# Kernel optimization log

Hardware: AMD Instinct MI355X
Metric: run time of the kernel (lower is better)

The kernel has to match this reference:

```python
import jax, jax.numpy as jnp
import numpy as np

N, E, D, H, FF = 50000, 800000, 128, 8, 512
DK = D // H
NTYPES = 5
EPS = 1e-5


def setup_inputs() -> dict:
    key = jax.random.key(0)
    ks = jax.random.split(key, 8)
    x = jax.random.normal(ks[0], (N, D), jnp.float32)
    edges = jax.random.randint(ks[1], (2, E), 0, N)
    etype = jax.random.randint(ks[2], (E,), 0, NTYPES)
    masks = etype[None, :] == jnp.arange(NTYPES)[:, None]  # [5, E] bool, exact partition
    s = 1.0 / np.sqrt(D)
    Wk = jax.random.normal(ks[3], (NTYPES, D, D), jnp.float32) * s
    bk = jnp.zeros((NTYPES, D), jnp.float32)
    ln1_g = jnp.ones((D,), jnp.float32)
    ln1_b = jnp.zeros((D,), jnp.float32)
    ln2_g = jnp.ones((D,), jnp.float32)
    ln2_b = jnp.zeros((D,), jnp.float32)
    W1 = jax.random.normal(ks[4], (D, FF), jnp.float32) * s
    b1 = jnp.zeros((FF,), jnp.float32)
    W2 = jax.random.normal(ks[5], (FF, D), jnp.float32) * (1.0 / np.sqrt(FF))
    b2 = jnp.zeros((D,), jnp.float32)
    return {"x": x, "edges": edges, "masks": masks, "Wk": Wk, "bk": bk,
            "ln1_g": ln1_g, "ln1_b": ln1_b, "ln2_g": ln2_g, "ln2_b": ln2_b,
            "W1": W1, "b1": b1, "W2": W2, "b2": b2}


def _layernorm(x, g, b):
    mu = x.mean(-1, keepdims=True)
    var = x.var(-1, keepdims=True)
    return (x - mu) * jax.lax.rsqrt(var + EPS) * g + b


def _proj(z, idx, masks, W, b):
    # per-edge-type masked linear: output[mask_i] = x[idx[mask_i]] @ W_i + b_i
    g = z[idx]  # [E, D] gather
    out = jnp.zeros((g.shape[0], D), z.dtype)
    for i in range(NTYPES):
        out = out + jnp.where(masks[i][:, None], g @ W[i] + b[i], 0.0)
    return out.reshape(-1, H, DK)  # [E, H, d_k]


def reference(x, edges, masks, Wk, bk, ln1_g, ln1_b, ln2_g, ln2_b, W1, b1, W2, b2):
    src, dst = edges[0], edges[1]
    n = x.shape[0]
    z = _layernorm(x, ln1_g, ln1_b)
    # source module uses self.key projection for query, key AND value
    q = _proj(z, src, masks, Wk, bk)   # [E, H, d_k]
    k = _proj(z, dst, masks, Wk, bk)   # [E, H, d_k]
    v = k                              # value = key(z, edges[1]) == key, reuse
    logits = (q * k).sum(2, keepdims=True)  # [E, H, 1], unscaled as in source
    m = jax.ops.segment_max(jax.lax.stop_gradient(logits), src, num_segments=n)
    scores = jnp.exp(logits - m[src])
    den = jax.ops.segment_sum(scores, src, num_segments=n)
    scores = scores / den[src]
    attn = jax.ops.segment_sum(scores * v, src, num_segments=n).reshape(n, -1)  # [N, D]
    x = x + attn
    z2 = _layernorm(x, ln2_g, ln2_b)
    ff = jax.nn.relu(z2 @ W1 + b1) @ W2 + b2
    return x + ff
```

## Files before the change

### kernel.cpp

```cpp
#include <hip/hip_runtime.h>

#define D 128
#define H 8
#define DK 16
#define FFDIM 512
#define NTYPES 5
#define LN_EPS 1e-5f

typedef __bf16 bf16x8 __attribute__((ext_vector_type(8)));
typedef float f32x4 __attribute__((ext_vector_type(4)));
typedef unsigned short ushort_t;
typedef unsigned int uint_t;

__device__ inline ushort_t bfbits(float f) {
  __bf16 b = (__bf16)f;
  return __builtin_bit_cast(ushort_t, b);
}

__global__ void detect_kernel(const unsigned char* __restrict__ m8, int E,
                              int* __restrict__ flag) {
  int lane = threadIdx.x;
  int s = 1;
  if (lane < E) {
    s = 0;
#pragma unroll
    for (int i = 0; i < NTYPES; ++i) s += (m8[(size_t)i * E + lane] != 0);
  }
  unsigned long long b = __ballot(s == 1);
  if (lane == 0) *flag = (b == ~0ull) ? 1 : 0;
}

__device__ inline int decode_etype(const unsigned char* __restrict__ m8,
                                   int E, int e, int is8) {
  int t = 0;
  if (is8) {
#pragma unroll
    for (int i = 1; i < NTYPES; ++i) t += i * (m8[(size_t)i * E + e] != 0);
  } else {
    const int* m32 = (const int*)m8;
#pragma unroll
    for (int i = 1; i < NTYPES; ++i) t += i * (m32[(size_t)i * E + e] != 0);
  }
  return t > (NTYPES - 1) ? (NTYPES - 1) : t;
}

__global__ void conv_frag_kernel(const float* __restrict__ W,
                                 ushort_t* __restrict__ hi,
                                 int K, int Ncol, size_t matW, size_t matF) {
  int gid = blockIdx.x * 256 + threadIdx.x;
  int total = (Ncol / 16) * (K / 32) * 64;
  if (gid >= total) return;
  const float* Wm = W + (size_t)blockIdx.y * matW;
  ushort_t* him = hi + (size_t)blockIdx.y * matF;
  int l = gid & 63;
  int ck = gid >> 6;
  int kk = ck % (K / 32);
  int c = ck / (K / 32);
  int row0 = kk * 32 + (l >> 4) * 8;
  int col = c * 16 + (l & 15);
  size_t ob = (size_t)gid * 8;
#pragma unroll
  for (int j = 0; j < 8; ++j) {
    float w = Wm[(size_t)(row0 + j) * Ncol + col];
    __bf16 h = (__bf16)w;
    him[ob + j] = __builtin_bit_cast(ushort_t, h);
  }
}

__global__ __launch_bounds__(256, 4) void projln_kernel(
    const float* __restrict__ x, const float* __restrict__ g,
    const float* __restrict__ b, const ushort_t* __restrict__ wkh,
    const float* __restrict__ bk, ushort_t* __restrict__ P, int n) {
  __shared__ ushort_t zsh[64 * D];
  __shared__ ushort_t zsl[64 * D];
  int tid = threadIdx.x, w = tid >> 6, l = tid & 63;
  int n0 = blockIdx.x * 64;

  for (int i = w; i < 64; i += 4) {
    int r = n0 + i;
    float v0 = 0.f, v1 = 0.f;
    if (r < n) {
      v0 = x[(size_t)r * D + l];
      v1 = x[(size_t)r * D + 64 + l];
    }
    float s = v0 + v1, ss = v0 * v0 + v1 * v1;
    for (int o = 32; o; o >>= 1) { s += __shfl_xor(s, o); ss += __shfl_xor(ss, o); }
    float mu = s * (1.f / D);
    float var = ss * (1.f / D) - mu * mu;
    float rs = rsqrtf(var + LN_EPS);
    float z0 = (v0 - mu) * rs * g[l] + b[l];
    float z1 = (v1 - mu) * rs * g[l + 64] + b[l + 64];
    int sw = (i & 7) << 3;
    int e0 = (i * D + l) ^ sw;
    int e1 = (i * D + l + 64) ^ sw;
    __bf16 h0 = (__bf16)z0, h1 = (__bf16)z1;
    zsh[e0] = __builtin_bit_cast(ushort_t, h0);
    zsh[e1] = __builtin_bit_cast(ushort_t, h1);
    __bf16 l0 = (__bf16)(z0 - (float)h0), l1 = (__bf16)(z1 - (float)h1);
    zsl[e0] = __builtin_bit_cast(ushort_t, l0);
    zsl[e1] = __builtin_bit_cast(ushort_t, l1);
  }
  __syncthreads();

  int lrow = w * 16 + (l & 15);
  int koff = (l >> 4) * 8;
  bf16x8 ah[4], al[4];
#pragma unroll
  for (int kk = 0; kk < 4; ++kk) {
    int e = (lrow * D + kk * 32 + koff) ^ ((lrow & 7) << 3);
    ah[kk] = *(const bf16x8*)(zsh + e);
    al[kk] = *(const bf16x8*)(zsl + e);
  }

  int col16 = l & 15, rgrp = (l >> 4) * 4;
  int rowbase = n0 + w * 16;
  for (int t = 0; t < NTYPES; ++t) {
    const ushort_t* bh0 = wkh + (size_t)t * (D * D);
    ushort_t* Pt = P + (size_t)t * n * D;
#pragma unroll
    for (int cp = 0; cp < 4; ++cp) {
      bf16x8 Bh[2][4];
#pragma unroll
      for (int cc = 0; cc < 2; ++cc)
#pragma unroll
        for (int kk = 0; kk < 4; ++kk) {
          size_t o = ((size_t)((cp * 2 + cc) * 4 + kk) * 64 + l) * 8;
          Bh[cc][kk] = *(const bf16x8*)(bh0 + o);
        }
      f32x4 aa[2], ac[2];
#pragma unroll
      for (int cc = 0; cc < 2; ++cc) {
        float bias = bk[t * D + (cp * 2 + cc) * 16 + col16];
        aa[cc] = (f32x4){bias, bias, bias, bias};
        ac[cc] = (f32x4){0.f, 0.f, 0.f, 0.f};
      }
#pragma unroll
      for (int kk = 0; kk < 4; ++kk)
#pragma unroll
        for (int cc = 0; cc < 2; ++cc) {
          aa[cc] = __builtin_amdgcn_mfma_f32_16x16x32_bf16(ah[kk], Bh[cc][kk], aa[cc], 0, 0, 0);
          ac[cc] = __builtin_amdgcn_mfma_f32_16x16x32_bf16(al[kk], Bh[cc][kk], ac[cc], 0, 0, 0);
        }
#pragma unroll
      for (int cc = 0; cc < 2; ++cc)
#pragma unroll
        for (int r = 0; r < 4; ++r) {
          int row = rowbase + rgrp + r;
          if (row < n)
            Pt[(size_t)row * D + (cp * 2 + cc) * 16 + col16] =
                bfbits(aa[cc][r] + ac[cc][r]);
        }
    }
  }
}

__global__ void zero_kernel(int* __restrict__ p, int n) {
  int i = blockIdx.x * 256 + threadIdx.x;
  if (i < n) p[i] = 0;
}

__global__ void hist5_kernel(const int* __restrict__ edges,
                             const unsigned char* __restrict__ masks,
                             const int* __restrict__ flag,
                             int* __restrict__ cnt5,
                             unsigned char* __restrict__ etype8, int E) {
  int e = blockIdx.x * 256 + threadIdx.x;
  if (e >= E) return;
  int t = decode_etype(masks, E, e, *flag);
  etype8[e] = (unsigned char)t;
  atomicAdd(&cnt5[edges[e] * 8 + t], 1);
}

__global__ __launch_bounds__(256) void scanA5_kernel(const int* __restrict__ cnt5,
                                                     int* __restrict__ loc,
                                                     int* __restrict__ bsums, int n) {
  __shared__ int ts[256];
  int tid = threadIdx.x;
  int i = blockIdx.x * 256 + tid;
  int v = 0;
  if (i < n) {
    int4 c0 = *(const int4*)(cnt5 + (size_t)i * 8);
    v = c0.x + c0.y + c0.z + c0.w + cnt5[(size_t)i * 8 + 4];
  }
  ts[tid] = v;
  __syncthreads();
  for (int o = 1; o < 256; o <<= 1) {
    int t = (tid >= o) ? ts[tid - o] : 0;
    __syncthreads();
    ts[tid] += t;
    __syncthreads();
  }
  if (i < n) loc[i] = ts[tid] - v;
  if (tid == 255) bsums[blockIdx.x] = ts[255];
}

__global__ __launch_bounds__(256) void scanB_kernel(int* __restrict__ bsums, int nb,
                                                    int* __restrict__ total) {
  __shared__ int ts[256];
  int tid = threadIdx.x;
  int per = (nb + 255) / 256;
  int start = tid * per;
  int end = min(start + per, nb);
  int s = 0;
  for (int i = start; i < end; ++i) s += bsums[i];
  ts[tid] = s;
  __syncthreads();
  for (int o = 1; o < 256; o <<= 1) {
    int t = (tid >= o) ? ts[tid - o] : 0;
    __syncthreads();
    ts[tid] += t;
    __syncthreads();
  }
  int run = ts[tid] - s;
  for (int i = start; i < end; ++i) {
    int v = bsums[i];
    bsums[i] = run;
    run += v;
  }
  if (tid == 255) *total = ts[255];
}

__global__ void build5_kernel(const int* __restrict__ loc,
                              const int* __restrict__ bsums,
                              const int* __restrict__ cnt5,
                              int* __restrict__ cursor5, int* __restrict__ tb,
                              int n) {
  int i = blockIdx.x * 256 + threadIdx.x;
  if (i >= n) return;
  int base = loc[i] + bsums[i >> 8];
#pragma unroll
  for (int t = 0; t < NTYPES; ++t) {
    int c = cnt5[(size_t)i * 8 + t];
    cursor5[(size_t)i * 8 + t] = base;
    tb[(size_t)i * 8 + t] = base;
    base += c;
  }
  tb[(size_t)i * 8 + 5] = base;
}

__global__ __launch_bounds__(256) void fill_kernel(
    const int* __restrict__ edges, const unsigned char* __restrict__ etype8,
    int* __restrict__ cursor5, int* __restrict__ elist, int E, int n) {
  int bx = blockIdx.x;
  int range = bx & 7;
  int e = (bx >> 3) * 256 + threadIdx.x;
  if (e >= E) return;
  int per = (n + 7) >> 3;
  int lo = range * per;
  int hi = min(lo + per, n);
  int src = edges[e];
  if (src < lo || src >= hi) return;
  int t = etype8[e];
  int dst = edges[E + e];
  int pos = atomicAdd(&cursor5[src * 8 + t], 1);
  elist[pos] = t * n + dst;
}

__global__ __launch_bounds__(256, 4) void attn_kernel(
    const float* __restrict__ x, const ushort_t* __restrict__ P,
    const int* __restrict__ tb, const int* __restrict__ elist,
    float* __restrict__ out, int n) {
  int node = (blockIdx.x * 256 + threadIdx.x) >> 4;
  int gl = threadIdx.x & 15;
  if (node >= n) return;

  int4 t03 = *(const int4*)(tb + (size_t)node * 8);
  int2 t45 = *(const int2*)(tb + (size_t)node * 8 + 4);
  int bnd0 = t03.x, bnd1 = t03.y, bnd2 = t03.z, bnd3 = t03.w;
  int bnd4 = t45.x, bnd5 = t45.y;

  float m = -1e30f, den = 0.f;
  float a[8];
#pragma unroll
  for (int i = 0; i < 8; ++i) a[i] = 0.f;

#pragma unroll
  for (int t = 0; t < NTYPES; ++t) {
    int jb = (t == 0) ? bnd0 : (t == 1) ? bnd1 : (t == 2) ? bnd2
             : (t == 3) ? bnd3 : bnd4;
    int je = (t == 0) ? bnd1 : (t == 1) ? bnd2 : (t == 2) ? bnd3
             : (t == 3) ? bnd4 : bnd5;
    if (jb >= je) continue;
    bf16x8 qb = *(const bf16x8*)(P + (size_t)(t * n + node) * D + gl * 8);
    float qf[8];
#pragma unroll
    for (int d = 0; d < 8; ++d) qf[d] = (float)qb[d];

    int row = elist[jb];
    bf16x8 kv = *(const bf16x8*)(P + (size_t)row * D + gl * 8);
    for (int j = jb; j < je; ++j) {
      bf16x8 kvn = kv;
      if (j + 1 < je) {
        int rn = elist[j + 1];
        kvn = *(const bf16x8*)(P + (size_t)rn * D + gl * 8);
      }
      float kf[8], p = 0.f;
#pragma unroll
      for (int d = 0; d < 8; ++d) {
        kf[d] = (float)kv[d];
        p += qf[d] * kf[d];
      }
      p += __shfl_xor(p, 1);
      float nm = fmaxf(m, p);
      float sc = __expf(m - nm);
      float w = __expf(p - nm);
      den = den * sc + w;
#pragma unroll
      for (int d = 0; d < 8; ++d) a[d] = a[d] * sc + w * kf[d];
      m = nm;
      kv = kvn;
    }
  }

  float inv = (bnd5 > bnd0) ? 1.f / den : 0.f;
  const float* xr = x + (size_t)node * D + gl * 8;
  float* orow = out + (size_t)node * D + gl * 8;
  float4 xa = *(const float4*)xr;
  float4 xb = *(const float4*)(xr + 4);
  float4 oa, ob;
  oa.x = xa.x + a[0] * inv; oa.y = xa.y + a[1] * inv;
  oa.z = xa.z + a[2] * inv; oa.w = xa.w + a[3] * inv;
  ob.x = xb.x + a[4] * inv; ob.y = xb.y + a[5] * inv;
  ob.z = xb.z + a[6] * inv; ob.w = xb.w + a[7] * inv;
  *(float4*)orow = oa;
  *(float4*)(orow + 4) = ob;
}

__global__ __launch_bounds__(256, 4) void ffn_mfma_kernel(
    const ushort_t* __restrict__ w1h, const ushort_t* __restrict__ w2h,
    const float* __restrict__ b1, const float* __restrict__ b2,
    const float* __restrict__ g, const float* __restrict__ bln,
    float* __restrict__ out, int n) {
  __shared__ char smem[16640 + 4 * 2304];
  ushort_t* z2h = (ushort_t*)smem;
  ushort_t* z2l = (ushort_t*)(smem + 8192);
  float* red = (float*)smem;
  int tid = threadIdx.x, w = tid >> 6, l = tid & 63;
  int n0 = blockIdx.x * 32;
  int r2 = w & 1, ph = w >> 1;
  float* hbw = (float*)(smem + 16640) + w * 576;

  for (int i = w; i < 32; i += 4) {
    int r = n0 + i;
    float v0 = 0.f, v1 = 0.f;
    if (r < n) {
      v0 = out[(size_t)r * D + l];
      v1 = out[(size_t)r * D + 64 + l];
    }
    float s = v0 + v1, ss = v0 * v0 + v1 * v1;
    for (int o = 32; o; o >>= 1) { s += __shfl_xor(s, o); ss += __shfl_xor(ss, o); }
    float mu = s * (1.f / D);
    float var = ss * (1.f / D) - mu * mu;
    float rs = rsqrtf(var + LN_EPS);
    float z0 = (v0 - mu) * rs * g[l] + bln[l];
    float z1 = (v1 - mu) * rs * g[l + 64] + bln[l + 64];
    int sw = (i & 7) << 3;
    int e0 = (i * D + l) ^ sw;
    int e1 = (i * D + l + 64) ^ sw;
    __bf16 h0 = (__bf16)z0, h1 = (__bf16)z1;
    z2h[e0] = __builtin_bit_cast(ushort_t, h0);
    z2h[e1] = __builtin_bit_cast(ushort_t, h1);
    __bf16 l0 = (__bf16)(z0 - (float)h0), l1 = (__bf16)(z1 - (float)h1);
    z2l[e0] = __builtin_bit_cast(ushort_t, l0);
    z2l[e1] = __builtin_bit_cast(ushort_t, l1);
  }
  __syncthreads();

  int lrow = r2 * 16 + (l & 15);
  int koff = (l >> 4) * 8;
  bf16x8 ah[4], al[4];
#pragma unroll
  for (int kk = 0; kk < 4; ++kk) {
    int e = (lrow * D + kk * 32 + koff) ^ ((lrow & 7) << 3);
    ah[kk] = *(const bf16x8*)(z2h + e);
    al[kk] = *(const bf16x8*)(z2l + e);
  }
  __syncthreads();

  int col16 = l & 15, rgrp = (l >> 4) * 4;
  f32x4 acc2[8];
#pragma unroll
  for (int c = 0; c < 8; ++c) acc2[c] = (f32x4){0.f, 0.f, 0.f, 0.f};

  for (int i = 0; i < 8; ++i) {
    int kk2 = 2 * i + ph;
    bf16x8 B1h[2][4];
#pragma unroll
    for (int cc = 0; cc < 2; ++cc)
#pragma unroll
      for (int kk = 0; kk < 4; ++kk) {
        size_t o = ((size_t)((kk2 * 2 + cc) * 4 + kk) * 64 + l) * 8;
        B1h[cc][kk] = *(const bf16x8*)(w1h + o);
      }
    f32x4 ha[2], hc[2];
#pragma unroll
    for (int cc = 0; cc < 2; ++cc) {
      float bias = b1[(kk2 * 2 + cc) * 16 + col16];
      ha[cc] = (f32x4){bias, bias, bias, bias};
      hc[cc] = (f32x4){0.f, 0.f, 0.f, 0.f};
    }
#pragma unroll
    for (int kk = 0; kk < 4; ++kk)
#pragma unroll
      for (int cc = 0; cc < 2; ++cc) {
        ha[cc] = __builtin_amdgcn_mfma_f32_16x16x32_bf16(ah[kk], B1h[cc][kk], ha[cc], 0, 0, 0);
        hc[cc] = __builtin_amdgcn_mfma_f32_16x16x32_bf16(al[kk], B1h[cc][kk], hc[cc], 0, 0, 0);
      }
#pragma unroll
    for (int cc = 0; cc < 2; ++cc)
#pragma unroll
      for (int r = 0; r < 4; ++r)
        hbw[(rgrp + r) * 36 + cc * 16 + col16] = fmaxf(ha[cc][r] + hc[cc][r], 0.f);
    float av[8];
    *(float4*)&av[0] = *(const float4*)&hbw[(l & 15) * 36 + koff];
    *(float4*)&av[4] = *(const float4*)&hbw[(l & 15) * 36 + koff + 4];
    bf16x8 a2h, a2l;
#pragma unroll
    for (int j = 0; j < 8; ++j) {
      __bf16 hv = (__bf16)av[j];
      a2h[j] = hv;
      a2l[j] = (__bf16)(av[j] - (float)hv);
    }
#pragma unroll
    for (int half = 0; half < 2; ++half) {
      bf16x8 B2h[4];
#pragma unroll
      for (int c2 = 0; c2 < 4; ++c2) {
        int ct = half * 4 + c2;
        size_t o = ((size_t)(ct * 16 + kk2) * 64 + l) * 8;
        B2h[c2] = *(const bf16x8*)(w2h + o);
      }
#pragma unroll
      for (int c2 = 0; c2 < 4; ++c2) {
        int ct = half * 4 + c2;
        acc2[ct] = __builtin_amdgcn_mfma_f32_16x16x32_bf16(a2h, B2h[c2], acc2[ct], 0, 0, 0);
        acc2[ct] = __builtin_amdgcn_mfma_f32_16x16x32_bf16(a2l, B2h[c2], acc2[ct], 0, 0, 0);
      }
    }
  }

  if (ph == 0) {
#pragma unroll
    for (int ct = 0; ct < 8; ++ct)
#pragma unroll
      for (int r = 0; r < 4; ++r)
        red[(r2 * 16 + rgrp + r) * 130 + ct * 16 + col16] = acc2[ct][r];
  }
  __syncthreads();
  if (ph == 1) {
#pragma unroll
    for (int ct = 0; ct < 8; ++ct) {
      int col = ct * 16 + col16;
      float bias2 = b2[col];
#pragma unroll
      for (int r = 0; r < 4; ++r) {
        int row = n0 + r2 * 16 + rgrp + r;
        if (row < n) {
          float part = red[(r2 * 16 + rgrp + r) * 130 + col];
          size_t o = (size_t)row * D + col;
          out[o] = out[o] + acc2[ct][r] + part + bias2;
        }
      }
    }
  }
}

extern "C" void kernel_launch(void* const* d_in, const int* in_sizes, int n_in,
                              void* d_out, int out_size, void* d_ws, size_t ws_size,
                              hipStream_t stream) {
  const float* x      = (const float*)d_in[0];
  const int* edges    = (const int*)d_in[1];
  const unsigned char* masks = (const unsigned char*)d_in[2];
  const float* Wk     = (const float*)d_in[3];
  const float* bk     = (const float*)d_in[4];
  const float* ln1_g  = (const float*)d_in[5];
  const float* ln1_b  = (const float*)d_in[6];
  const float* ln2_g  = (const float*)d_in[7];
  const float* ln2_b  = (const float*)d_in[8];
  const float* W1     = (const float*)d_in[9];
  const float* b1     = (const float*)d_in[10];
  const float* W2     = (const float*)d_in[11];
  const float* b2     = (const float*)d_in[12];
  float* out = (float*)d_out;

  const int n = in_sizes[0] / D;
  const int E = in_sizes[1] / 2;
  const int nbn = (n + 255) / 256;

  char* ws = (char*)d_ws;
  size_t off = 0;
  ushort_t* P = (ushort_t*)(ws + off);  off += (size_t)NTYPES * n * D * sizeof(ushort_t);
  int* cnt5   = (int*)(ws + off);       off += (size_t)n * 8 * sizeof(int);
  int* cursor5= (int*)(ws + off);       off += (size_t)n * 8 * sizeof(int);
  int* tb     = (int*)(ws + off);       off += (size_t)n * 8 * sizeof(int);
  int* loc    = (int*)(ws + off);       off += (size_t)n * sizeof(int);
  int* bsums  = (int*)(ws + off);       off += (size_t)nbn * sizeof(int);
  int* total  = (int*)(ws + off);       off += 64;
  int* elist  = (int*)(ws + off);       off += (size_t)E * sizeof(int);
  unsigned char* etype8 = (unsigned char*)(ws + off); off += (size_t)E + 64;
  int* flag   = (int*)(ws + off);       off += 64;
  ushort_t* wkh = (ushort_t*)(ws + off); off += (size_t)NTYPES * D * D * sizeof(ushort_t);
  ushort_t* w1h = (ushort_t*)(ws + off); off += (size_t)D * FFDIM * sizeof(ushort_t);
  ushort_t* w2h = (ushort_t*)(ws + off); off += (size_t)FFDIM * D * sizeof(ushort_t);
  (void)ws_size; (void)n_in; (void)out_size;

  detect_kernel<<<1, 64, 0, stream>>>(masks, E, flag);

  {
    dim3 gwk((8 * 4 * 64 + 255) / 256, NTYPES);
    conv_frag_kernel<<<gwk, 256, 0, stream>>>(Wk, wkh, D, D,
                                              (size_t)D * D, (size_t)D * D);
    dim3 gw1(((FFDIM / 16) * 4 * 64 + 255) / 256, 1);
    conv_frag_kernel<<<gw1, 256, 0, stream>>>(W1, w1h, D, FFDIM, 0, 0);
    dim3 gw2((8 * (FFDIM / 32) * 64 + 255) / 256, 1);
    conv_frag_kernel<<<gw2, 256, 0, stream>>>(W2, w2h, FFDIM, D, 0, 0);
  }

  projln_kernel<<<(n + 63) / 64, 256, 0, stream>>>(x, ln1_g, ln1_b, wkh, bk, P, n);

  zero_kernel<<<(n * 8 + 255) / 256, 256, 0, stream>>>(cnt5, n * 8);
  hist5_kernel<<<(E + 255) / 256, 256, 0, stream>>>(edges, masks, flag, cnt5, etype8, E);
  scanA5_kernel<<<nbn, 256, 0, stream>>>(cnt5, loc, bsums, n);
  scanB_kernel<<<1, 256, 0, stream>>>(bsums, nbn, total);
  build5_kernel<<<(n + 255) / 256, 256, 0, stream>>>(loc, bsums, cnt5, cursor5, tb, n);
  fill_kernel<<<((E + 255) / 256) * 8, 256, 0, stream>>>(edges, etype8, cursor5,
                                                         elist, E, n);

  attn_kernel<<<(n + 15) / 16, 256, 0, stream>>>(x, P, tb, elist, out, n);

  ffn_mfma_kernel<<<(n + 31) / 32, 256, 0, stream>>>(w1h, w2h,
                                                     b1, b2, ln2_g, ln2_b, out, n);
}
```

Baseline: 244.0 us.

## Drop bf16 split-precision in FFN and range-partition the edge histogram

The FFN kernel no longer splits the LayerNorm and ReLU activations into high and low bf16 halves. It runs a single bf16 MFMA per tile, which halves the matrix-core work and removes some shared-memory traffic. Separately, edge-type decoding moves into its own kernel, and the histogram is launched with 8 times as many blocks, each handling only the edges whose source node falls in one eighth of the node range. This is meant to localise atomic contention and improve L2 locality. The cost is lower FFN accuracy, with bf16 activations only, and reading the edge list 8 times.

After: 242.2 us. Within noise of the previous version (-0.7%).

```diff
diff --git a/kernel.cpp b/kernel.cpp
--- a/kernel.cpp
+++ b/kernel.cpp
@@ -159,16 +159,27 @@
   if (i < n) p[i] = 0;
 }
 
-__global__ void hist5_kernel(const int* __restrict__ edges,
-                             const unsigned char* __restrict__ masks,
+__global__ void etype_kernel(const unsigned char* __restrict__ masks,
                              const int* __restrict__ flag,
-                             int* __restrict__ cnt5,
                              unsigned char* __restrict__ etype8, int E) {
   int e = blockIdx.x * 256 + threadIdx.x;
   if (e >= E) return;
-  int t = decode_etype(masks, E, e, *flag);
-  etype8[e] = (unsigned char)t;
-  atomicAdd(&cnt5[edges[e] * 8 + t], 1);
+  etype8[e] = (unsigned char)decode_etype(masks, E, e, *flag);
+}
+
+__global__ __launch_bounds__(256) void hist5_kernel(
+    const int* __restrict__ edges, const unsigned char* __restrict__ etype8,
+    int* __restrict__ cnt5, int E, int n) {
+  int bx = blockIdx.x;
+  int range = bx & 7;
+  int e = (bx >> 3) * 256 + threadIdx.x;
+  if (e >= E) return;
+  int per = (n + 7) >> 3;
+  int lo = range * per;
+  int hi = min(lo + per, n);
+  int src = edges[e];
+  if (src < lo || src >= hi) return;
+  atomicAdd(&cnt5[src * 8 + etype8[e]], 1);
 }
 
 __global__ __launch_bounds__(256) void scanA5_kernel(const int* __restrict__ cnt5,
@@ -333,7 +344,6 @@
     float* __restrict__ out, int n) {
   __shared__ char smem[16640 + 4 * 2304];
   ushort_t* z2h = (ushort_t*)smem;
-  ushort_t* z2l = (ushort_t*)(smem + 8192);
   float* red = (float*)smem;
   int tid = threadIdx.x, w = tid >> 6, l = tid & 63;
   int n0 = blockIdx.x * 32;
@@ -360,20 +370,16 @@
     __bf16 h0 = (__bf16)z0, h1 = (__bf16)z1;
     z2h[e0] = __builtin_bit_cast(ushort_t, h0);
     z2h[e1] = __builtin_bit_cast(ushort_t, h1);
-    __bf16 l0 = (__bf16)(z0 - (float)h0), l1 = (__bf16)(z1 - (float)h1);
-    z2l[e0] = __builtin_bit_cast(ushort_t, l0);
-    z2l[e1] = __builtin_bit_cast(ushort_t, l1);
   }
   __syncthreads();
 
   int lrow = r2 * 16 + (l & 15);
   int koff = (l >> 4) * 8;
-  bf16x8 ah[4], al[4];
+  bf16x8 ah[4];
 #pragma unroll
   for (int kk = 0; kk < 4; ++kk) {
     int e = (lrow * D + kk * 32 + koff) ^ ((lrow & 7) << 3);
     ah[kk] = *(const bf16x8*)(z2h + e);
-    al[kk] = *(const bf16x8*)(z2l + e);
   }
   __syncthreads();
 
@@ -392,35 +398,28 @@
         size_t o = ((size_t)((kk2 * 2 + cc) * 4 + kk) * 64 + l) * 8;
         B1h[cc][kk] = *(const bf16x8*)(w1h + o);
       }
-    f32x4 ha[2], hc[2];
+    f32x4 ha[2];
 #pragma unroll
     for (int cc = 0; cc < 2; ++cc) {
       float bias = b1[(kk2 * 2 + cc) * 16 + col16];
       ha[cc] = (f32x4){bias, bias, bias, bias};
-      hc[cc] = (f32x4){0.f, 0.f, 0.f, 0.f};
     }
 #pragma unroll
     for (int kk = 0; kk < 4; ++kk)
 #pragma unroll
-      for (int cc = 0; cc < 2; ++cc) {
+      for (int cc = 0; cc < 2; ++cc)
         ha[cc] = __builtin_amdgcn_mfma_f32_16x16x32_bf16(ah[kk], B1h[cc][kk], ha[cc], 0, 0, 0);
-        hc[cc] = __builtin_amdgcn_mfma_f32_16x16x32_bf16(al[kk], B1h[cc][kk], hc[cc], 0, 0, 0);
-      }
 #pragma unroll
     for (int cc = 0; cc < 2; ++cc)
 #pragma unroll
       for (int r = 0; r < 4; ++r)
-        hbw[(rgrp + r) * 36 + cc * 16 + col16] = fmaxf(ha[cc][r] + hc[cc][r], 0.f);
+        hbw[(rgrp + r) * 36 + cc * 16 + col16] = fmaxf(ha[cc][r], 0.f);
     float av[8];
     *(float4*)&av[0] = *(const float4*)&hbw[(l & 15) * 36 + koff];
     *(float4*)&av[4] = *(const float4*)&hbw[(l & 15) * 36 + koff + 4];
-    bf16x8 a2h, a2l;
-#pragma unroll
-    for (int j = 0; j < 8; ++j) {
-      __bf16 hv = (__bf16)av[j];
-      a2h[j] = hv;
-      a2l[j] = (__bf16)(av[j] - (float)hv);
-    }
+    bf16x8 a2h;
+#pragma unroll
+    for (int j = 0; j < 8; ++j) a2h[j] = (__bf16)av[j];
 #pragma unroll
     for (int half = 0; half < 2; ++half) {
       bf16x8 B2h[4];
@@ -434,7 +433,6 @@
       for (int c2 = 0; c2 < 4; ++c2) {
         int ct = half * 4 + c2;
         acc2[ct] = __builtin_amdgcn_mfma_f32_16x16x32_bf16(a2h, B2h[c2], acc2[ct], 0, 0, 0);
-        acc2[ct] = __builtin_amdgcn_mfma_f32_16x16x32_bf16(a2l, B2h[c2], acc2[ct], 0, 0, 0);
       }
     }
   }
@@ -519,7 +517,8 @@
   projln_kernel<<<(n + 63) / 64, 256, 0, stream>>>(x, ln1_g, ln1_b, wkh, bk, P, n);
 
   zero_kernel<<<(n * 8 + 255) / 256, 256, 0, stream>>>(cnt5, n * 8);
-  hist5_kernel<<<(E + 255) / 256, 256, 0, stream>>>(edges, masks, flag, cnt5, etype8, E);
+  etype_kernel<<<(E + 255) / 256, 256, 0, stream>>>(masks, flag, etype8, E);
+  hist5_kernel<<<((E + 255) / 256) * 8, 256, 0, stream>>>(edges, etype8, cnt5, E, n);
   scanA5_kernel<<<nbn, 256, 0, stream>>>(cnt5, loc, bsums, n);
   scanB_kernel<<<1, 256, 0, stream>>>(bsums, nbn, total);
   build5_kernel<<<(n + 255) / 256, 256, 0, stream>>>(loc, bsums, cnt5, cursor5, tb, n);
```
